# Optimization experiments

Measured on AMD Instinct MI355X. Metric: run time of the kernel, lower is better.

## Reference

```python
import jax, jax.numpy as jnp
import numpy as np

EPS = 1e-8


def setup_inputs() -> dict:
    key = jax.random.key(0)
    k1, k2 = jax.random.split(key)
    B, C, L = 16, 4, 4096
    K, S = 256, 128
    x = jax.random.normal(k1, (B, C, L), dtype=jnp.float32)
    shapelets = jax.random.normal(k2, (C, K, S), dtype=jnp.float32)
    return {"x": x, "shapelets": shapelets}


def reference(x, shapelets):
    # x: (B, C, L); shapelets: (C, K, S)
    B, C, L = x.shape
    _, K, S = shapelets.shape
    W = L - S + 1  # number of sliding windows

    # unfold: (B, C, W, S) sliding windows with stride 1
    idx = jnp.arange(W)[:, None] + jnp.arange(S)[None, :]  # (W, S)
    win = x[:, :, idx]  # (B, C, W, S)
    win = win / jnp.maximum(jnp.linalg.norm(win, axis=-1, keepdims=True), EPS)

    shp = shapelets / jnp.maximum(
        jnp.linalg.norm(shapelets, axis=-1, keepdims=True), EPS
    )  # (C, K, S)

    # pairwise dot products: (B, C, W, K)
    sim = jnp.einsum("bcws,cks->bcwk", win, shp)
    # sum over channels, keepdim, transpose(2,3), divide by n_dims
    sim = jnp.sum(sim, axis=1, keepdims=True) / C  # (B, 1, W, K)
    sim = jnp.transpose(sim, (0, 1, 3, 2))  # (B, 1, K, W)
    sim = jax.nn.relu(sim)
    # global max-pool over window positions -> (B, 1, K)
    return jnp.max(sim, axis=3)
```

## Files before the change

kernel.cpp:

```cpp
#include <hip/hip_runtime.h>
#include <hip/hip_bf16.h>

#define NB 16
#define NC 4
#define NL 4096
#define NK 256
#define NS 128
#define NW (NL - NS + 1)
#define WPB 128
#define NWT ((NW + WPB - 1) / WPB)
#define EPSF 1e-8f

typedef __attribute__((ext_vector_type(8))) short bf16x8;
typedef __attribute__((ext_vector_type(4))) float floatx4;

__device__ inline short f2bf(float f) {
    __hip_bfloat16 h = __float2bfloat16(f);
    short s;
    __builtin_memcpy(&s, &h, sizeof(short));
    return s;
}

__global__ __launch_bounds__(64)
void norm_shp_kernel(const float* __restrict__ shp, short* __restrict__ shpn) {
    int ck = blockIdx.x;
    int lane = threadIdx.x;
    const float* p = shp + (size_t)ck * NS;
    float v0 = p[lane];
    float v1 = p[lane + 64];
    float ss = v0 * v0 + v1 * v1;
    #pragma unroll
    for (int o = 32; o > 0; o >>= 1) ss += __shfl_xor(ss, o, 64);
    float rn = 1.f / fmaxf(sqrtf(ss), EPSF);
    shpn[(size_t)ck * NS + lane]      = f2bf(v0 * rn);
    shpn[(size_t)ck * NS + lane + 64] = f2bf(v1 * rn);
}

__global__ __launch_bounds__(256, 2)
void mcs_main_kernel(const float* __restrict__ x,
                     const short* __restrict__ shpn,
                     float* __restrict__ partial) {
    __shared__ bf16x8 bs[NK * 16];
    __shared__ float xs[NC][WPB + NS];
    __shared__ float invs[NC][WPB];
    __shared__ float red[4][NK];

    const int wt = blockIdx.x, b = blockIdx.y;
    const int w0 = wt * WPB;
    const int tid = threadIdx.x;

    float xv[4];
    #pragma unroll
    for (int i = 0; i < 4; i++) {
        int idx = tid + 256 * i;
        int c = idx >> 8, o = idx & 255;
        int g = w0 + o;
        xv[i] = (g < NL) ? x[((size_t)b * NC + c) * NL + g] : 0.f;
    }
    bf16x8 breg[16];
    {
        const bf16x8* p = (const bf16x8*)shpn;
        #pragma unroll
        for (int i = 0; i < 16; i++) breg[i] = p[i * 256 + tid];
    }
    #pragma unroll
    for (int i = 0; i < 4; i++) {
        int idx = tid + 256 * i;
        xs[idx >> 8][idx & 255] = xv[i];
    }
    __syncthreads();
    #pragma unroll
    for (int i = 0; i < 2; i++) {
        int idx = tid + 256 * i;
        int c = idx >> 7, o = idx & 127;
        const float* p = &xs[c][o];
        float ss = 0.f;
        #pragma unroll 4
        for (int s = 0; s < NS; s++) { float v = p[s]; ss += v * v; }
        int w = w0 + o;
        invs[c][o] = (w < NW) ? 1.f / fmaxf(sqrtf(ss), EPSF) : 0.f;
    }
    #pragma unroll
    for (int i = 0; i < 16; i++) {
        int g = i * 256 + tid;
        int k = g >> 4, cc = g & 15;
        bs[(k << 4) | (cc ^ (k & 15))] = breg[i];
    }
    __syncthreads();

    const int lane = tid & 63, wv = tid >> 6;
    const int m = lane & 15, q = lane >> 4;

    floatx4 acc[2][16];
    #pragma unroll
    for (int mt = 0; mt < 2; mt++)
        #pragma unroll
        for (int t = 0; t < 16; t++) acc[mt][t] = (floatx4){0.f, 0.f, 0.f, 0.f};

    for (int c = 0; c < NC; c++) {
        if (c < NC - 1) {
            const bf16x8* p = (const bf16x8*)(shpn + (size_t)(c + 1) * NK * NS);
            #pragma unroll
            for (int i = 0; i < 16; i++) breg[i] = p[i * 256 + tid];
        }
        const float im0 = invs[c][wv * 32 + m];
        const float im1 = invs[c][wv * 32 + 16 + m];
        const float* xr0 = &xs[c][wv * 32 + m];
        #pragma unroll
        for (int s0 = 0; s0 < NS; s0 += 32) {
            bf16x8 a0, a1;
            #pragma unroll
            for (int j = 0; j < 8; j++) {
                a0[j] = f2bf(xr0[s0 + q * 8 + j] * im0);
                a1[j] = f2bf(xr0[16 + s0 + q * 8 + j] * im1);
            }
            const int base = (m << 4) | (((s0 >> 3) + q) ^ m);
            #pragma unroll
            for (int t = 0; t < 16; t++) {
                bf16x8 bf = bs[t * 256 + base];
                acc[0][t] = __builtin_amdgcn_mfma_f32_16x16x32_bf16(a0, bf, acc[0][t], 0, 0, 0);
                acc[1][t] = __builtin_amdgcn_mfma_f32_16x16x32_bf16(a1, bf, acc[1][t], 0, 0, 0);
            }
        }
        if (c < NC - 1) {
            __syncthreads();
            #pragma unroll
            for (int i = 0; i < 16; i++) {
                int g = i * 256 + tid;
                int k = g >> 4, cc = g & 15;
                bs[(k << 4) | (cc ^ (k & 15))] = breg[i];
            }
            __syncthreads();
        }
    }

    #pragma unroll
    for (int t = 0; t < 16; t++) {
        floatx4 v0 = acc[0][t], v1 = acc[1][t];
        float mx = fmaxf(fmaxf(fmaxf(v0.x, v0.y), fmaxf(v0.z, v0.w)),
                         fmaxf(fmaxf(v1.x, v1.y), fmaxf(v1.z, v1.w)));
        mx = fmaxf(mx, __shfl_xor(mx, 16, 64));
        mx = fmaxf(mx, __shfl_xor(mx, 32, 64));
        if (lane < 16) red[wv][t * 16 + lane] = mx;
    }
    __syncthreads();
    if (tid < NK) {
        float p0 = fmaxf(fmaxf(red[0][tid], red[1][tid]), fmaxf(red[2][tid], red[3][tid]));
        partial[((size_t)b * NWT + wt) * NK + tid] = p0;
    }
}

__global__ __launch_bounds__(256)
void finalize_kernel(const float* __restrict__ partial, float* __restrict__ out) {
    int b = blockIdx.x, k = threadIdx.x;
    float mx = 0.f;
    for (int wtile = 0; wtile < NWT; wtile++)
        mx = fmaxf(mx, partial[((size_t)b * NWT + wtile) * NK + k]);
    out[(size_t)b * NK + k] = 0.25f * mx;
}

extern "C" void kernel_launch(void* const* d_in, const int* in_sizes, int n_in,
                              void* d_out, int out_size, void* d_ws, size_t ws_size,
                              hipStream_t stream) {
    (void)in_sizes; (void)n_in; (void)out_size; (void)ws_size;
    const float* x   = (const float*)d_in[0];
    const float* shp = (const float*)d_in[1];
    float* out = (float*)d_out;

    char* ws = (char*)d_ws;
    short* shpn    = (short*)ws;
    float* partial = (float*)(ws + 262144);

    norm_shp_kernel<<<NC * NK, 64, 0, stream>>>(shp, shpn);
    mcs_main_kernel<<<dim3(NWT, NB), 256, 0, stream>>>(x, shpn, partial);
    finalize_kernel<<<NB, 256, 0, stream>>>(partial, out);
}
```

Before: 79.97 us.

## Retile MFMA warps to 4x8, use prefix-sum norms and atomic finalize

Each wave now computes a 64-window by 128-shapelet tile, so every B fragment read from LDS feeds four MFMAs instead of two. Window norms come from a prefix sum of squares instead of a 128-step serial loop per thread. x is kept in LDS as bf16 in four shifted copies so A fragments load with aligned 8-byte reads. The separate finalize kernel is replaced by an atomicMax on the output. The atomicMax relies on the output starting at zero, since no memset is issued. Rounding x to bf16 before normalising, and taking norms as differences of prefix sums, both add a small amount of numerical error.

```diff
diff --git a/kernel.cpp b/kernel.cpp
--- a/kernel.cpp
+++ b/kernel.cpp
@@ -39,23 +39,22 @@
 __global__ __launch_bounds__(256, 2)
 void mcs_main_kernel(const float* __restrict__ x,
                      const short* __restrict__ shpn,
-                     float* __restrict__ partial) {
+                     float* __restrict__ out) {
     __shared__ bf16x8 bs[NK * 16];
-    __shared__ float xs[NC][WPB + NS];
+    __shared__ alignas(16) short xcp[NC][4][264];
+    __shared__ alignas(16) float scratch[NC][264];
     __shared__ float invs[NC][WPB];
-    __shared__ float red[4][NK];
 
     const int wt = blockIdx.x, b = blockIdx.y;
     const int w0 = wt * WPB;
     const int tid = threadIdx.x;
-
-    float xv[4];
-    #pragma unroll
-    for (int i = 0; i < 4; i++) {
-        int idx = tid + 256 * i;
-        int c = idx >> 8, o = idx & 255;
-        int g = w0 + o;
-        xv[i] = (g < NL) ? x[((size_t)b * NC + c) * NL + g] : 0.f;
+    const int lane = tid & 63, wv = tid >> 6;
+
+    float xv[NC];
+    #pragma unroll
+    for (int c = 0; c < NC; c++) {
+        int g = w0 + tid;
+        xv[c] = (g < NL) ? x[((size_t)b * NC + c) * NL + g] : 0.f;
     }
     bf16x8 breg[16];
     {
@@ -64,21 +63,29 @@
         for (int i = 0; i < 16; i++) breg[i] = p[i * 256 + tid];
     }
     #pragma unroll
-    for (int i = 0; i < 4; i++) {
-        int idx = tid + 256 * i;
-        xs[idx >> 8][idx & 255] = xv[i];
-    }
-    __syncthreads();
-    #pragma unroll
-    for (int i = 0; i < 2; i++) {
-        int idx = tid + 256 * i;
-        int c = idx >> 7, o = idx & 127;
-        const float* p = &xs[c][o];
-        float ss = 0.f;
-        #pragma unroll 4
-        for (int s = 0; s < NS; s++) { float v = p[s]; ss += v * v; }
-        int w = w0 + o;
-        invs[c][o] = (w < NW) ? 1.f / fmaxf(sqrtf(ss), EPSF) : 0.f;
+    for (int c = 0; c < NC; c++) {
+        short hv = f2bf(xv[c]);
+        #pragma unroll
+        for (int r = 0; r < 4; r++) {
+            int o2 = tid - r;
+            if (o2 >= 0) xcp[c][r][o2] = hv;
+        }
+        scratch[c][tid] = xv[c] * xv[c];
+    }
+    __syncthreads();
+
+    {
+        float4 v = *(const float4*)&scratch[wv][lane * 4];
+        v.y += v.x; v.z += v.y; v.w += v.z;
+        float tot = v.w;
+        #pragma unroll
+        for (int o = 1; o < 64; o <<= 1) {
+            float u = __shfl_up(tot, o, 64);
+            if (lane >= o) tot += u;
+        }
+        float excl = tot - v.w;
+        v.x += excl; v.y += excl; v.z += excl; v.w += excl;
+        *(float4*)&scratch[wv][lane * 4] = v;
     }
     #pragma unroll
     for (int i = 0; i < 16; i++) {
@@ -88,38 +95,62 @@
     }
     __syncthreads();
 
-    const int lane = tid & 63, wv = tid >> 6;
+    #pragma unroll
+    for (int i = 0; i < 2; i++) {
+        int idx = tid + 256 * i;
+        int c = idx >> 7, o = idx & 127;
+        float nn = scratch[c][o + 127] - (o ? scratch[c][o - 1] : 0.f);
+        int w = w0 + o;
+        invs[c][o] = (w < NW) ? 1.f / fmaxf(sqrtf(fmaxf(nn, 0.f)), EPSF) : 0.f;
+    }
+    __syncthreads();
+
     const int m = lane & 15, q = lane >> 4;
-
-    floatx4 acc[2][16];
-    #pragma unroll
-    for (int mt = 0; mt < 2; mt++)
-        #pragma unroll
-        for (int t = 0; t < 16; t++) acc[mt][t] = (floatx4){0.f, 0.f, 0.f, 0.f};
-
+    const int kh = wv & 1, wh = wv >> 1;
+
+    floatx4 acc[4][8];
+    #pragma unroll
+    for (int mt = 0; mt < 4; mt++)
+        #pragma unroll
+        for (int kt = 0; kt < 8; kt++) acc[mt][kt] = (floatx4){0.f, 0.f, 0.f, 0.f};
+
+    const int r = m & 3;
     for (int c = 0; c < NC; c++) {
         if (c < NC - 1) {
             const bf16x8* p = (const bf16x8*)(shpn + (size_t)(c + 1) * NK * NS);
             #pragma unroll
             for (int i = 0; i < 16; i++) breg[i] = p[i * 256 + tid];
         }
-        const float im0 = invs[c][wv * 32 + m];
-        const float im1 = invs[c][wv * 32 + 16 + m];
-        const float* xr0 = &xs[c][wv * 32 + m];
+        float im[4];
+        #pragma unroll
+        for (int mt = 0; mt < 4; mt++) im[mt] = invs[c][wh * 64 + mt * 16 + m];
+
         #pragma unroll
         for (int s0 = 0; s0 < NS; s0 += 32) {
-            bf16x8 a0, a1;
-            #pragma unroll
-            for (int j = 0; j < 8; j++) {
-                a0[j] = f2bf(xr0[s0 + q * 8 + j] * im0);
-                a1[j] = f2bf(xr0[16 + s0 + q * 8 + j] * im1);
+            bf16x8 a[4];
+            #pragma unroll
+            for (int mt = 0; mt < 4; mt++) {
+                int tt = wh * 64 + mt * 16 + m + s0 + q * 8;
+                const uint2* pp = (const uint2*)&xcp[c][r][tt - r];
+                uint2 u0 = pp[0], u1 = pp[1];
+                float imv = im[mt];
+                a[mt][0] = f2bf(__uint_as_float(u0.x << 16) * imv);
+                a[mt][1] = f2bf(__uint_as_float(u0.x & 0xffff0000u) * imv);
+                a[mt][2] = f2bf(__uint_as_float(u0.y << 16) * imv);
+                a[mt][3] = f2bf(__uint_as_float(u0.y & 0xffff0000u) * imv);
+                a[mt][4] = f2bf(__uint_as_float(u1.x << 16) * imv);
+                a[mt][5] = f2bf(__uint_as_float(u1.x & 0xffff0000u) * imv);
+                a[mt][6] = f2bf(__uint_as_float(u1.y << 16) * imv);
+                a[mt][7] = f2bf(__uint_as_float(u1.y & 0xffff0000u) * imv);
             }
-            const int base = (m << 4) | (((s0 >> 3) + q) ^ m);
-            #pragma unroll
-            for (int t = 0; t < 16; t++) {
-                bf16x8 bf = bs[t * 256 + base];
-                acc[0][t] = __builtin_amdgcn_mfma_f32_16x16x32_bf16(a0, bf, acc[0][t], 0, 0, 0);
-                acc[1][t] = __builtin_amdgcn_mfma_f32_16x16x32_bf16(a1, bf, acc[1][t], 0, 0, 0);
+            int cc = (s0 >> 3) + q;
+            #pragma unroll
+            for (int kt = 0; kt < 8; kt++) {
+                int k = kh * 128 + kt * 16 + m;
+                bf16x8 bf = bs[(k << 4) | (cc ^ m)];
+                #pragma unroll
+                for (int mt = 0; mt < 4; mt++)
+                    acc[mt][kt] = __builtin_amdgcn_mfma_f32_16x16x32_bf16(a[mt], bf, acc[mt][kt], 0, 0, 0);
             }
         }
         if (c < NC - 1) {
@@ -134,29 +165,26 @@
         }
     }
 
-    #pragma unroll
-    for (int t = 0; t < 16; t++) {
-        floatx4 v0 = acc[0][t], v1 = acc[1][t];
+    __syncthreads();
+    #pragma unroll
+    for (int kt = 0; kt < 8; kt++) {
+        floatx4 v0 = acc[0][kt], v1 = acc[1][kt], v2 = acc[2][kt], v3 = acc[3][kt];
         float mx = fmaxf(fmaxf(fmaxf(v0.x, v0.y), fmaxf(v0.z, v0.w)),
                          fmaxf(fmaxf(v1.x, v1.y), fmaxf(v1.z, v1.w)));
+        mx = fmaxf(mx, fmaxf(fmaxf(fmaxf(v2.x, v2.y), fmaxf(v2.z, v2.w)),
+                             fmaxf(fmaxf(v3.x, v3.y), fmaxf(v3.z, v3.w))));
         mx = fmaxf(mx, __shfl_xor(mx, 16, 64));
         mx = fmaxf(mx, __shfl_xor(mx, 32, 64));
-        if (lane < 16) red[wv][t * 16 + lane] = mx;
-    }
-    __syncthreads();
-    if (tid < NK) {
-        float p0 = fmaxf(fmaxf(red[0][tid], red[1][tid]), fmaxf(red[2][tid], red[3][tid]));
-        partial[((size_t)b * NWT + wt) * NK + tid] = p0;
-    }
-}
-
-__global__ __launch_bounds__(256)
-void finalize_kernel(const float* __restrict__ partial, float* __restrict__ out) {
-    int b = blockIdx.x, k = threadIdx.x;
-    float mx = 0.f;
-    for (int wtile = 0; wtile < NWT; wtile++)
-        mx = fmaxf(mx, partial[((size_t)b * NWT + wtile) * NK + k]);
-    out[(size_t)b * NK + k] = 0.25f * mx;
+        if (lane < 16) scratch[wv][kt * 16 + lane] = mx;
+    }
+    __syncthreads();
+    {
+        int k = tid;
+        int khh = k >> 7, lk = k & 127;
+        float v = fmaxf(scratch[khh][lk], scratch[khh + 2][lk]);
+        v = fmaxf(v, 0.f) * 0.25f;
+        atomicMax((int*)out + (size_t)b * NK + k, __float_as_int(v));
+    }
 }
 
 extern "C" void kernel_launch(void* const* d_in, const int* in_sizes, int n_in,
@@ -167,11 +195,8 @@
     const float* shp = (const float*)d_in[1];
     float* out = (float*)d_out;
 
-    char* ws = (char*)d_ws;
-    short* shpn    = (short*)ws;
-    float* partial = (float*)(ws + 262144);
+    short* shpn = (short*)d_ws;
 
     norm_shp_kernel<<<NC * NK, 64, 0, stream>>>(shp, shpn);
-    mcs_main_kernel<<<dim3(NWT, NB), 256, 0, stream>>>(x, shpn, partial);
-    finalize_kernel<<<NB, 256, 0, stream>>>(partial, out);
-}
+    mcs_main_kernel<<<dim3(NWT, NB), 256, 0, stream>>>(x, shpn, out);
+}
```

After: 79.97 us. About the same (-0.0%).
